# Optimization experiments

Hardware: AMD Instinct MI355X
Metric: run time of the kernel (lower is better)

## Reference

```python
import jax, jax.numpy as jnp
import numpy as np

TEMP = 0.01            # entropy temperature
THRESH = 0.92          # hamming similarity threshold
BETA = 0.25            # commitment weight
ENT_W = 0.1            # entropy loss weight


def _l2_normalize(x, axis=-1, eps=1e-12):
    n = jnp.sqrt(jnp.sum(x * x, axis=axis, keepdims=True))
    return x / jnp.maximum(n, eps)


def _entropy_loss(affinity):
    # affinity: [N, K] codebook affinities (cosine similarities)
    fa = affinity / TEMP
    probs = jax.nn.softmax(fa, axis=-1)
    log_probs = jax.nn.log_softmax(fa + 1e-5, axis=-1)
    avg_probs = jnp.mean(probs, axis=0)
    avg_entropy = -jnp.sum(avg_probs * jnp.log(avg_probs + 1e-5))
    sample_entropy = -jnp.mean(jnp.sum(probs * log_probs, axis=-1))
    return sample_entropy - avg_entropy


def _hamming_consistency_loss(input_blocks, z_e):
    # binary occupancy: non-air voxels -> 1
    binary = (jnp.argmax(input_blocks, axis=1) != 0).astype(jnp.float32)  # [B,24,24,24]
    B = binary.shape[0]
    # faithful to torch: plain reshapes (no transpose)
    patterns = binary.reshape(B, 6, 4, 6, 4, 6, 4).reshape(B, 6, 6, 6, 64).reshape(-1, 64)
    N = patterns.shape[0]
    P = patterns
    # pairwise hamming distance via two Gram matmuls
    ham = P @ (1.0 - P).T + (1.0 - P) @ P.T          # [N,N]
    sim = 1.0 - ham / 64.0
    mask = (sim > THRESH) & (~jnp.eye(N, dtype=bool))
    W = jax.lax.stop_gradient(jnp.where(mask, sim, 0.0))  # detached weights
    # pre-quant embeddings per chunk, l2-normalized; cosine distance matrix
    emb = jnp.transpose(z_e, (0, 2, 3, 4, 1)).reshape(N, -1)  # [N, C]
    en = _l2_normalize(emb, axis=1)
    cos = en @ en.T                                   # [N,N]
    dist = 1.0 - cos
    return jnp.sum(dist * W) / (jnp.sum(W) + 1e-8)


def setup_inputs() -> dict:
    key = jax.random.key(0)
    k1, k2, k3 = jax.random.split(key, 3)
    input_blocks = jax.random.normal(k1, (16, 32, 24, 24, 24), dtype=jnp.float32)
    z_e = jax.random.normal(k2, (16, 256, 6, 6, 6), dtype=jnp.float32)
    codebook = jax.random.normal(k3, (1024, 256), dtype=jnp.float32)
    return {"input_blocks": input_blocks, "z_e": z_e, "codebook": codebook}


def reference(input_blocks, z_e, codebook):
    B, C, H, W, D = z_e.shape
    z = jnp.transpose(z_e, (0, 2, 3, 4, 1)).reshape(-1, C)   # [N, C]
    zn = _l2_normalize(z, axis=1)
    en = _l2_normalize(codebook, axis=1)                      # [K, C]
    affinity = zn @ en.T                                      # [N, K]
    idx = jnp.argmax(affinity, axis=1)                        # max cosine == min L2 on sphere
    z_q = en[idx]                                             # [N, C]
    sg = jax.lax.stop_gradient
    codebook_loss = jnp.mean((z_q - sg(zn)) ** 2)
    commit_loss = BETA * jnp.mean((sg(z_q) - zn) ** 2)
    ent_loss = ENT_W * _entropy_loss(affinity)
    ham_loss = _hamming_consistency_loss(input_blocks, z_e)
    loss = codebook_loss + commit_loss + ent_loss + ham_loss
    # straight-through estimator
    z_q_ste = zn + sg(z_q - zn)
    z_q_out = jnp.transpose(z_q_ste.reshape(B, H, W, D, C), (0, 4, 1, 2, 3))
    return z_q_out, loss, idx
```

## Files before the change

### kernel.cpp

```cpp
#include <hip/hip_runtime.h>
#include <cstdint>
#include <cstddef>

#define N_ROWS 3456
#define C_DIM 256
#define K_CB 1024
#define B_SZ 16
#define SPATIAL 216
#define VOX 13824
#define NCH 32
#define NSB 216

typedef __attribute__((ext_vector_type(16))) float f32x16;
typedef __attribute__((ext_vector_type(8))) short bf16x8;

__device__ __forceinline__ unsigned short f2bf_rne(float f) {
    unsigned int u = __float_as_uint(f);
    u += 0x7FFFu + ((u >> 16) & 1u);
    return (unsigned short)(u >> 16);
}
__device__ __forceinline__ float bf2f(unsigned short h) {
    unsigned int u = ((unsigned int)h) << 16;
    return __uint_as_float(u);
}

__device__ __forceinline__ size_t swz(int n, int c) {
    return (size_t)(n >> 5) * 8192 + (size_t)((c >> 3) * 256) + (size_t)((n & 31) * 8) + (c & 7);
}

__global__ __launch_bounds__(256) void k_pre(
        const float* __restrict__ in, const float* __restrict__ cb,
        const float* __restrict__ ze,
        unsigned long long* __restrict__ pats,
        float* __restrict__ scal,
        float* __restrict__ en,
        unsigned short* __restrict__ ehi, unsigned short* __restrict__ elo,
        unsigned short* __restrict__ zhi, unsigned short* __restrict__ zlo) {
    int bid = blockIdx.x;
    int t = threadIdx.x;
    if (bid < 864) {
        if (bid == 0 && t < 16) scal[t] = 0.0f;
        int v = bid * 256 + t;
        int b = v / VOX;
        int r = v % VOX;
        const float* p = in + (size_t)b * NCH * VOX + r;
        float v0 = p[0];
        float mx = -INFINITY;
#pragma unroll
        for (int c = 1; c < NCH; ++c) mx = fmaxf(mx, p[(size_t)c * VOX]);
        unsigned long long m = __ballot(mx > v0);
        if ((t & 63) == 0) pats[v >> 6] = m;
        return;
    }
    __shared__ float ws[4];
    if (bid < 1888) {
        int k = bid - 864, c = t;
        float v = cb[k * C_DIM + c];
        float ss = v * v;
#pragma unroll
        for (int off = 32; off > 0; off >>= 1) ss += __shfl_down(ss, off, 64);
        if ((c & 63) == 0) ws[c >> 6] = ss;
        __syncthreads();
        float nrm = fmaxf(sqrtf(ws[0] + ws[1] + ws[2] + ws[3]), 1e-12f);
        float o = v / nrm;
        en[k * C_DIM + c] = o;
        unsigned short h = f2bf_rne(o);
        size_t off = swz(k, c);
        ehi[off] = h;
        elo[off] = f2bf_rne(o - bf2f(h));
    } else {
        int n = bid - 1888, c = t;
        int b = n / SPATIAL, s = n % SPATIAL;
        float v = ze[((size_t)(b * C_DIM + c)) * SPATIAL + s];
        float ss = v * v;
#pragma unroll
        for (int off = 32; off > 0; off >>= 1) ss += __shfl_down(ss, off, 64);
        if ((c & 63) == 0) ws[c >> 6] = ss;
        __syncthreads();
        float nrm = fmaxf(sqrtf(ws[0] + ws[1] + ws[2] + ws[3]), 1e-12f);
        float o = v / nrm;
        unsigned short h = f2bf_rne(o);
        size_t off = swz(n, c);
        zhi[off] = h;
        zlo[off] = f2bf_rne(o - bf2f(h));
    }
}

__global__ __launch_bounds__(128) void k_mid(
        const unsigned short* __restrict__ zhi, const unsigned short* __restrict__ zlo,
        const unsigned short* __restrict__ ehi, const unsigned short* __restrict__ elo,
        const unsigned long long* __restrict__ pats,
        float* __restrict__ aff, float* __restrict__ scal) {
    int t = threadIdx.x;
    int w = t >> 6, lane = t & 63;
    int bid = blockIdx.x;
    const bf16x8* __restrict__ Zh = (const bf16x8*)zhi;
    const bf16x8* __restrict__ Zl = (const bf16x8*)zlo;
    const bf16x8* __restrict__ Eh = (const bf16x8*)ehi;
    const bf16x8* __restrict__ El = (const bf16x8*)elo;

    if (bid < 432) {
        int ib = bid % 54, jb = bid / 54;
        int i0 = ib * 64, j0 = jb * 128;
        int sa = ib * 2;
        int sb = jb * 4 + w * 2;

        f32x16 acc[2][2];
#pragma unroll
        for (int r = 0; r < 2; ++r)
#pragma unroll
            for (int q = 0; q < 2; ++q)
#pragma unroll
                for (int e = 0; e < 16; ++e) acc[r][q][e] = 0.0f;

#pragma unroll
        for (int s16 = 0; s16 < 16; ++s16) {
            int u = s16 * 64 + lane;
            bf16x8 ah[2], al[2], bh[2], bl[2];
#pragma unroll
            for (int r = 0; r < 2; ++r) {
                ah[r] = Zh[(size_t)(sa + r) * 1024 + u];
                al[r] = Zl[(size_t)(sa + r) * 1024 + u];
            }
#pragma unroll
            for (int q = 0; q < 2; ++q) {
                bh[q] = Eh[(size_t)(sb + q) * 1024 + u];
                bl[q] = El[(size_t)(sb + q) * 1024 + u];
            }
#pragma unroll
            for (int r = 0; r < 2; ++r)
#pragma unroll
                for (int q = 0; q < 2; ++q) {
                    acc[r][q] = __builtin_amdgcn_mfma_f32_32x32x16_bf16(ah[r], bh[q], acc[r][q], 0, 0, 0);
                    acc[r][q] = __builtin_amdgcn_mfma_f32_32x32x16_bf16(ah[r], bl[q], acc[r][q], 0, 0, 0);
                    acc[r][q] = __builtin_amdgcn_mfma_f32_32x32x16_bf16(al[r], bh[q], acc[r][q], 0, 0, 0);
                }
        }
#pragma unroll
        for (int r = 0; r < 2; ++r)
#pragma unroll
            for (int q = 0; q < 2; ++q)
#pragma unroll
                for (int g = 0; g < 16; ++g) {
                    int row = i0 + r * 32 + (g & 3) + 8 * (g >> 2) + 4 * (lane >> 5);
                    int col = j0 + w * 64 + q * 32 + (lane & 31);
                    aff[(size_t)row * K_CB + col] = acc[r][q][g];
                }
        return;
    }

    int hb = bid - 432;
    int ti = 0, rem = hb;
    while (rem >= 27 - ti) { rem -= 27 - ti; ++ti; }
    int tj = ti + rem;
    int i0 = ti * 128, j0 = tj * 128;
    float factor = (ti == tj) ? 1.0f : 2.0f;
    int si = ti * 4 + w * 2;
    int sj = tj * 4;

    f32x16 acc[2][4];
#pragma unroll
    for (int a = 0; a < 2; ++a)
#pragma unroll
        for (int b = 0; b < 4; ++b)
#pragma unroll
            for (int e = 0; e < 16; ++e) acc[a][b][e] = 0.0f;

#pragma unroll
    for (int s16 = 0; s16 < 16; ++s16) {
        int u = s16 * 64 + lane;
        bf16x8 a0 = Zh[(size_t)si * 1024 + u];
        bf16x8 a1 = Zh[(size_t)(si + 1) * 1024 + u];
        bf16x8 bf[4];
#pragma unroll
        for (int c = 0; c < 4; ++c)
            bf[c] = Zh[(size_t)(sj + c) * 1024 + u];
#pragma unroll
        for (int c = 0; c < 4; ++c) {
            acc[0][c] = __builtin_amdgcn_mfma_f32_32x32x16_bf16(a0, bf[c], acc[0][c], 0, 0, 0);
            acc[1][c] = __builtin_amdgcn_mfma_f32_32x32x16_bf16(a1, bf[c], acc[1][c], 0, 0, 0);
        }
    }

    unsigned long long pj[4];
#pragma unroll
    for (int c = 0; c < 4; ++c) pj[c] = pats[j0 + c * 32 + (lane & 31)];

    float sW = 0.0f, sD = 0.0f;
#pragma unroll
    for (int r = 0; r < 2; ++r) {
        int ibase = i0 + w * 64 + r * 32 + 4 * (lane >> 5);
#pragma unroll
        for (int g = 0; g < 16; ++g) {
            int gi = ibase + (g & 3) + 8 * (g >> 2);
            unsigned long long pi = pats[gi];
#pragma unroll
            for (int c = 0; c < 4; ++c) {
                int gj = j0 + c * 32 + (lane & 31);
                int pop = __popcll(pi ^ pj[c]);
                float wgt = (pop <= 5 && gi != gj) ? (1.0f - (float)pop * 0.015625f) : 0.0f;
                sW += wgt;
                sD += wgt * acc[r][c][g];
            }
        }
    }
#pragma unroll
    for (int off = 32; off > 0; off >>= 1) {
        sW += __shfl_down(sW, off, 64);
        sD += __shfl_down(sD, off, 64);
    }
    if (lane == 0) {
        atomicAdd(&scal[2], factor * sW);
        atomicAdd(&scal[3], factor * sD);
    }
}

#define ZQS 257
__global__ __launch_bounds__(1024) void k_post(
        const float* __restrict__ aff, const float* __restrict__ en,
        float* __restrict__ avgp_part, float* __restrict__ scal,
        float* __restrict__ out) {
    __shared__ float lps[16][K_CB];
    __shared__ float zq[16 * ZQS];
    __shared__ float lsc[32];
    __shared__ float ws16[16];
    __shared__ int lastflag;
    unsigned int* done = (unsigned int*)&scal[8];
    int t = threadIdx.x;
    int lane = t & 63, w = t >> 6;
    int n0 = blockIdx.x * 16;
    int row = n0 + w;

    const float* ap = aff + (size_t)row * K_CB;
    float4 v[4];
#pragma unroll
    for (int j = 0; j < 4; ++j)
        v[j] = *(const float4*)&ap[j * 256 + lane * 4];

    float m = v[0].x; int mi = lane * 4;
#pragma unroll
    for (int j = 0; j < 4; ++j)
#pragma unroll
        for (int i = 0; i < 4; ++i) {
            float x = ((const float*)&v[j])[i];
            int col = j * 256 + lane * 4 + i;
            if (x > m) { m = x; mi = col; }
        }
#pragma unroll
    for (int off = 32; off > 0; off >>= 1) {
        float vo = __shfl_down(m, off, 64);
        int   io = __shfl_down(mi, off, 64);
        if (vo > m || (vo == m && io < mi)) { m = vo; mi = io; }
    }
    m = __shfl(m, 0, 64);
    mi = __shfl(mi, 0, 64);

    float e[16];
    float S = 0.0f, T = 0.0f;
#pragma unroll
    for (int j = 0; j < 4; ++j)
#pragma unroll
        for (int i = 0; i < 4; ++i) {
            float d = 100.0f * (((const float*)&v[j])[i] - m);
            float ee = __expf(d);
            e[j * 4 + i] = ee; S += ee; T += ee * d;
        }
#pragma unroll
    for (int off = 32; off > 0; off >>= 1) {
        S += __shfl_down(S, off, 64);
        T += __shfl_down(T, off, 64);
    }
    S = __shfl(S, 0, 64);
    T = __shfl(T, 0, 64);
    float invS = 1.0f / S;
    float se = logf(S) - T * invS;
    float cm = 2.0f - 2.0f * m;
    if (lane == 0) out[884737 + row] = (float)mi;

    float4 g4 = *(const float4*)&en[(size_t)mi * C_DIM + lane * 4];
    zq[w * ZQS + lane * 4 + 0] = g4.x;
    zq[w * ZQS + lane * 4 + 1] = g4.y;
    zq[w * ZQS + lane * 4 + 2] = g4.z;
    zq[w * ZQS + lane * 4 + 3] = g4.w;

#pragma unroll
    for (int j = 0; j < 4; ++j)
#pragma unroll
        for (int i = 0; i < 4; ++i)
            lps[w][j * 256 + lane * 4 + i] = e[j * 4 + i] * invS;
    if (lane == 0) { lsc[w] = se; lsc[16 + w] = cm; }
    __syncthreads();

    {
        float csum = 0.0f;
#pragma unroll
        for (int ww = 0; ww < 16; ++ww) csum += lps[ww][t];
        avgp_part[(size_t)blockIdx.x * K_CB + t] = csum;
    }
    if (t == 0) {
        float a = 0.0f;
#pragma unroll
        for (int i = 0; i < 16; ++i) a += lsc[i];
        atomicAdd(&scal[0], a);
    }
    if (t == 1) {
        float a = 0.0f;
#pragma unroll
        for (int i = 0; i < 16; ++i) a += lsc[16 + i];
        atomicAdd(&scal[1], a);
    }

    {
        int rlane = t & 15, cgrp = t >> 4;
        int n = n0 + rlane;
        int b = n / SPATIAL, s = n - b * SPATIAL;
        size_t obase = ((size_t)b * C_DIM) * SPATIAL + s;
#pragma unroll
        for (int cc = 0; cc < 4; ++cc) {
            int c = cgrp * 4 + cc;
            out[obase + (size_t)c * SPATIAL] = zq[rlane * ZQS + c];
        }
    }

    __syncthreads();
    if (t == 0) {
        __threadfence();
        unsigned int old = atomicAdd(done, 1u);
        lastflag = (old == NSB - 1) ? 1 : 0;
    }
    __syncthreads();
    if (lastflag) {
        __threadfence();
        float apv = 0.0f;
        for (int bb = 0; bb < NSB; ++bb)
            apv += avgp_part[(size_t)bb * K_CB + t];
        float ap2 = apv * (1.0f / N_ROWS);
        float term = ap2 * logf(ap2 + 1e-5f);
#pragma unroll
        for (int off = 32; off > 0; off >>= 1) term += __shfl_down(term, off, 64);
        if (lane == 0) ws16[w] = term;
        __syncthreads();
        if (t == 0) {
            float sAP = 0.0f;
#pragma unroll
            for (int i = 0; i < 16; ++i) sAP += ws16[i];
            float s0 = atomicAdd(&scal[0], 0.0f);
            float s1 = atomicAdd(&scal[1], 0.0f);
            float s2 = atomicAdd(&scal[2], 0.0f);
            float s3 = atomicAdd(&scal[3], 0.0f);
            float sample = s0 * (1.0f / N_ROWS);
            float commit = s1 * (1.0f / ((float)N_ROWS * C_DIM));
            float ent = 0.1f * (sample + sAP);
            float ham = (s2 - s3) / (s2 + 1e-8f);
            out[884736] = 1.25f * commit + ent + ham;
        }
    }
}

extern "C" void kernel_launch(void* const* d_in, const int* in_sizes, int n_in,
                              void* d_out, int out_size, void* d_ws, size_t ws_size,
                              hipStream_t stream) {
    const float* in_blocks = (const float*)d_in[0];
    const float* z_e       = (const float*)d_in[1];
    const float* cb        = (const float*)d_in[2];
    float* out = (float*)d_out;

    char* ws = (char*)d_ws;
    float* en   = (float*)(ws + 0);
    float* aff  = (float*)(ws + 1048576);
    unsigned short* zhi = (unsigned short*)(ws + 15204352);
    unsigned short* zlo = (unsigned short*)(ws + 16973824);
    unsigned short* ehi = (unsigned short*)(ws + 18743296);
    unsigned short* elo = (unsigned short*)(ws + 19267584);
    unsigned long long* pats = (unsigned long long*)(ws + 19791872);
    float* avgp_part = (float*)(ws + 19819520);
    float* scal = (float*)(ws + 20704256);

    k_pre<<<5344, 256, 0, stream>>>(in_blocks, cb, z_e, pats, scal,
                                    en, ehi, elo, zhi, zlo);
    k_mid<<<810, 128, 0, stream>>>(zhi, zlo, ehi, elo, pats, aff, scal);
    k_post<<<NSB, 1024, 0, stream>>>(aff, en, avgp_part, scal, out);
}
```

Before: 148.4 us.

## Fuse affinity GEMM with argmax/softmax epilogue, drop affinity buffer round-trip

Merges the affinity GEMM and the post-processing kernel into one launch. Each GEMM block now computes 32 rows against the full 1024-entry codebook across 8 waves, then does argmax, softmax statistics, the column sums for the average probabilities and the z_q scatter straight from registers. This removes the 14 MB affinity write and re-read and one kernel launch. In exchange there are fewer, larger GEMM blocks (108) at 512 threads with more register pressure, and the Hamming blocks leave 6 of their 8 waves idle.

```diff
diff --git a/kernel.cpp b/kernel.cpp
--- a/kernel.cpp
+++ b/kernel.cpp
@@ -9,7 +9,8 @@
 #define SPATIAL 216
 #define VOX 13824
 #define NCH 32
-#define NSB 216
+#define N_GBLK 108
+#define N_FBLK 486
 
 typedef __attribute__((ext_vector_type(16))) float f32x16;
 typedef __attribute__((ext_vector_type(8))) short bf16x8;
@@ -86,239 +87,245 @@
     }
 }
 
-__global__ __launch_bounds__(128) void k_mid(
+__global__ __launch_bounds__(512, 2) void k_fat(
         const unsigned short* __restrict__ zhi, const unsigned short* __restrict__ zlo,
         const unsigned short* __restrict__ ehi, const unsigned short* __restrict__ elo,
         const unsigned long long* __restrict__ pats,
-        float* __restrict__ aff, float* __restrict__ scal) {
+        const float* __restrict__ en,
+        float* __restrict__ avgp_part, float* __restrict__ scal,
+        float* __restrict__ out) {
+    __shared__ float zq[32 * 257];
+    __shared__ float sm[32][8];
+    __shared__ int   si[32][8];
+    __shared__ float sS[32][8];
+    __shared__ float sT[32][8];
+    __shared__ float gm[32];
+    __shared__ int   gmi[32];
+    __shared__ float invS[32];
+    __shared__ float ws8[8];
+    __shared__ int lastflag;
+    unsigned int* done = (unsigned int*)&scal[8];
+
     int t = threadIdx.x;
     int w = t >> 6, lane = t & 63;
+    int half = lane >> 5, l31 = lane & 31;
     int bid = blockIdx.x;
     const bf16x8* __restrict__ Zh = (const bf16x8*)zhi;
     const bf16x8* __restrict__ Zl = (const bf16x8*)zlo;
     const bf16x8* __restrict__ Eh = (const bf16x8*)ehi;
     const bf16x8* __restrict__ El = (const bf16x8*)elo;
 
-    if (bid < 432) {
-        int ib = bid % 54, jb = bid / 54;
-        int i0 = ib * 64, j0 = jb * 128;
-        int sa = ib * 2;
-        int sb = jb * 4 + w * 2;
-
-        f32x16 acc[2][2];
-#pragma unroll
-        for (int r = 0; r < 2; ++r)
-#pragma unroll
-            for (int q = 0; q < 2; ++q)
-#pragma unroll
-                for (int e = 0; e < 16; ++e) acc[r][q][e] = 0.0f;
+    if (bid < N_GBLK) {
+        int sa = bid;
+        int n0 = bid * 32;
+
+        f32x16 acc[4];
+#pragma unroll
+        for (int q = 0; q < 4; ++q)
+#pragma unroll
+            for (int e = 0; e < 16; ++e) acc[q][e] = 0.0f;
 
 #pragma unroll
         for (int s16 = 0; s16 < 16; ++s16) {
             int u = s16 * 64 + lane;
-            bf16x8 ah[2], al[2], bh[2], bl[2];
-#pragma unroll
-            for (int r = 0; r < 2; ++r) {
-                ah[r] = Zh[(size_t)(sa + r) * 1024 + u];
-                al[r] = Zl[(size_t)(sa + r) * 1024 + u];
-            }
-#pragma unroll
-            for (int q = 0; q < 2; ++q) {
-                bh[q] = Eh[(size_t)(sb + q) * 1024 + u];
-                bl[q] = El[(size_t)(sb + q) * 1024 + u];
-            }
-#pragma unroll
-            for (int r = 0; r < 2; ++r)
-#pragma unroll
-                for (int q = 0; q < 2; ++q) {
-                    acc[r][q] = __builtin_amdgcn_mfma_f32_32x32x16_bf16(ah[r], bh[q], acc[r][q], 0, 0, 0);
-                    acc[r][q] = __builtin_amdgcn_mfma_f32_32x32x16_bf16(ah[r], bl[q], acc[r][q], 0, 0, 0);
-                    acc[r][q] = __builtin_amdgcn_mfma_f32_32x32x16_bf16(al[r], bh[q], acc[r][q], 0, 0, 0);
+            bf16x8 ah = Zh[(size_t)sa * 1024 + u];
+            bf16x8 al = Zl[(size_t)sa * 1024 + u];
+            bf16x8 bh[4], bl[4];
+#pragma unroll
+            for (int q = 0; q < 4; ++q) {
+                bh[q] = Eh[(size_t)(w * 4 + q) * 1024 + u];
+                bl[q] = El[(size_t)(w * 4 + q) * 1024 + u];
+            }
+#pragma unroll
+            for (int q = 0; q < 4; ++q) {
+                acc[q] = __builtin_amdgcn_mfma_f32_32x32x16_bf16(ah, bh[q], acc[q], 0, 0, 0);
+                acc[q] = __builtin_amdgcn_mfma_f32_32x32x16_bf16(ah, bl[q], acc[q], 0, 0, 0);
+                acc[q] = __builtin_amdgcn_mfma_f32_32x32x16_bf16(al, bh[q], acc[q], 0, 0, 0);
+            }
+        }
+
+#pragma unroll
+        for (int g = 0; g < 16; ++g) {
+            float m = acc[0][g];
+            int mi = w * 128 + l31;
+#pragma unroll
+            for (int q = 1; q < 4; ++q) {
+                float x = acc[q][g];
+                int c = w * 128 + q * 32 + l31;
+                if (x > m) { m = x; mi = c; }
+            }
+#pragma unroll
+            for (int mask = 1; mask < 32; mask <<= 1) {
+                float vo = __shfl_xor(m, mask, 64);
+                int   io = __shfl_xor(mi, mask, 64);
+                if (vo > m || (vo == m && io < mi)) { m = vo; mi = io; }
+            }
+            int row = (g & 3) + 8 * (g >> 2) + 4 * half;
+            if (l31 == 0) { sm[row][w] = m; si[row][w] = mi; }
+        }
+        __syncthreads();
+
+        float cmv = 0.0f;
+        if (t < 32) {
+            float m = sm[t][0];
+            int mi = si[t][0];
+#pragma unroll
+            for (int ww = 1; ww < 8; ++ww) {
+                float mw = sm[t][ww];
+                int miw = si[t][ww];
+                if (mw > m || (mw == m && miw < mi)) { m = mw; mi = miw; }
+            }
+            gm[t] = m; gmi[t] = mi;
+            out[884737 + n0 + t] = (float)mi;
+            cmv = 2.0f - 2.0f * m;
+        }
+        if (w == 0) {
+#pragma unroll
+            for (int off = 32; off > 0; off >>= 1) cmv += __shfl_down(cmv, off, 64);
+            if (lane == 0) atomicAdd(&scal[1], cmv);
+        }
+        __syncthreads();
+
+#pragma unroll
+        for (int g = 0; g < 16; ++g) {
+            int row = (g & 3) + 8 * (g >> 2) + 4 * half;
+            float gmr = gm[row];
+            float S = 0.0f, T = 0.0f;
+#pragma unroll
+            for (int q = 0; q < 4; ++q) {
+                float d = 100.0f * (acc[q][g] - gmr);
+                float ee = __expf(d);
+                S += ee; T += ee * d;
+                acc[q][g] = ee;
+            }
+#pragma unroll
+            for (int mask = 1; mask < 32; mask <<= 1) {
+                S += __shfl_xor(S, mask, 64);
+                T += __shfl_xor(T, mask, 64);
+            }
+            if (l31 == 0) { sS[row][w] = S; sT[row][w] = T; }
+        }
+#pragma unroll
+        for (int rr = 0; rr < 4; ++rr) {
+            int row = w * 4 + rr;
+            int mi = gmi[row];
+            float4 g4 = *(const float4*)&en[(size_t)mi * C_DIM + lane * 4];
+            zq[row * 257 + lane * 4 + 0] = g4.x;
+            zq[row * 257 + lane * 4 + 1] = g4.y;
+            zq[row * 257 + lane * 4 + 2] = g4.z;
+            zq[row * 257 + lane * 4 + 3] = g4.w;
+        }
+        __syncthreads();
+
+        float sev = 0.0f;
+        if (t < 32) {
+            float S = 0.0f, T = 0.0f;
+#pragma unroll
+            for (int ww = 0; ww < 8; ++ww) { S += sS[t][ww]; T += sT[t][ww]; }
+            float iv = 1.0f / S;
+            invS[t] = iv;
+            sev = logf(S) - T * iv;
+        }
+        if (w == 0) {
+#pragma unroll
+            for (int off = 32; off > 0; off >>= 1) sev += __shfl_down(sev, off, 64);
+            if (lane == 0) atomicAdd(&scal[0], sev);
+        }
+        __syncthreads();
+
+        {
+            float cs[4] = {0.0f, 0.0f, 0.0f, 0.0f};
+#pragma unroll
+            for (int g = 0; g < 16; ++g) {
+                int row = (g & 3) + 8 * (g >> 2) + 4 * half;
+                float iv = invS[row];
+#pragma unroll
+                for (int q = 0; q < 4; ++q) cs[q] += acc[q][g] * iv;
+            }
+#pragma unroll
+            for (int q = 0; q < 4; ++q) cs[q] += __shfl_xor(cs[q], 32, 64);
+            if (half == 0) {
+#pragma unroll
+                for (int q = 0; q < 4; ++q)
+                    avgp_part[(size_t)bid * K_CB + w * 128 + q * 32 + l31] = cs[q];
+            }
+        }
+
+        {
+            int rl = t & 31, cg = t >> 5;
+            int n = n0 + rl;
+            int b = n / SPATIAL, s = n - b * SPATIAL;
+            size_t obase = ((size_t)b * C_DIM) * SPATIAL + s;
+#pragma unroll
+            for (int cc = 0; cc < 16; ++cc) {
+                int c = cg * 16 + cc;
+                out[obase + (size_t)c * SPATIAL] = zq[rl * 257 + c];
+            }
+        }
+    } else if (w < 2) {
+        int hb = bid - N_GBLK;
+        int ti = 0, rem = hb;
+        while (rem >= 27 - ti) { rem -= 27 - ti; ++ti; }
+        int tj = ti + rem;
+        int i0 = ti * 128, j0 = tj * 128;
+        float factor = (ti == tj) ? 1.0f : 2.0f;
+        int sib = ti * 4 + w * 2;
+        int sjb = tj * 4;
+
+        f32x16 acc[2][4];
+#pragma unroll
+        for (int a = 0; a < 2; ++a)
+#pragma unroll
+            for (int b = 0; b < 4; ++b)
+#pragma unroll
+                for (int e = 0; e < 16; ++e) acc[a][b][e] = 0.0f;
+
+#pragma unroll
+        for (int s16 = 0; s16 < 16; ++s16) {
+            int u = s16 * 64 + lane;
+            bf16x8 a0 = Zh[(size_t)sib * 1024 + u];
+            bf16x8 a1 = Zh[(size_t)(sib + 1) * 1024 + u];
+            bf16x8 bf[4];
+#pragma unroll
+            for (int c = 0; c < 4; ++c)
+                bf[c] = Zh[(size_t)(sjb + c) * 1024 + u];
+#pragma unroll
+            for (int c = 0; c < 4; ++c) {
+                acc[0][c] = __builtin_amdgcn_mfma_f32_32x32x16_bf16(a0, bf[c], acc[0][c], 0, 0, 0);
+                acc[1][c] = __builtin_amdgcn_mfma_f32_32x32x16_bf16(a1, bf[c], acc[1][c], 0, 0, 0);
+            }
+        }
+
+        unsigned long long pj[4];
+#pragma unroll
+        for (int c = 0; c < 4; ++c) pj[c] = pats[j0 + c * 32 + l31];
+
+        float sW = 0.0f, sD = 0.0f;
+#pragma unroll
+        for (int r = 0; r < 2; ++r) {
+            int ibase = i0 + w * 64 + r * 32 + 4 * half;
+#pragma unroll
+            for (int g = 0; g < 16; ++g) {
+                int gi = ibase + (g & 3) + 8 * (g >> 2);
+                unsigned long long pi = pats[gi];
+#pragma unroll
+                for (int c = 0; c < 4; ++c) {
+                    int gj = j0 + c * 32 + l31;
+                    int pop = __popcll(pi ^ pj[c]);
+                    float wgt = (pop <= 5 && gi != gj) ? (1.0f - (float)pop * 0.015625f) : 0.0f;
+                    sW += wgt;
+                    sD += wgt * acc[r][c][g];
                 }
-        }
-#pragma unroll
-        for (int r = 0; r < 2; ++r)
-#pragma unroll
-            for (int q = 0; q < 2; ++q)
-#pragma unroll
-                for (int g = 0; g < 16; ++g) {
-                    int row = i0 + r * 32 + (g & 3) + 8 * (g >> 2) + 4 * (lane >> 5);
-                    int col = j0 + w * 64 + q * 32 + (lane & 31);
-                    aff[(size_t)row * K_CB + col] = acc[r][q][g];
-                }
-        return;
-    }
-
-    int hb = bid - 432;
-    int ti = 0, rem = hb;
-    while (rem >= 27 - ti) { rem -= 27 - ti; ++ti; }
-    int tj = ti + rem;
-    int i0 = ti * 128, j0 = tj * 128;
-    float factor = (ti == tj) ? 1.0f : 2.0f;
-    int si = ti * 4 + w * 2;
-    int sj = tj * 4;
-
-    f32x16 acc[2][4];
-#pragma unroll
-    for (int a = 0; a < 2; ++a)
-#pragma unroll
-        for (int b = 0; b < 4; ++b)
-#pragma unroll
-            for (int e = 0; e < 16; ++e) acc[a][b][e] = 0.0f;
-
-#pragma unroll
-    for (int s16 = 0; s16 < 16; ++s16) {
-        int u = s16 * 64 + lane;
-        bf16x8 a0 = Zh[(size_t)si * 1024 + u];
-        bf16x8 a1 = Zh[(size_t)(si + 1) * 1024 + u];
-        bf16x8 bf[4];
-#pragma unroll
-        for (int c = 0; c < 4; ++c)
-            bf[c] = Zh[(size_t)(sj + c) * 1024 + u];
-#pragma unroll
-        for (int c = 0; c < 4; ++c) {
-            acc[0][c] = __builtin_amdgcn_mfma_f32_32x32x16_bf16(a0, bf[c], acc[0][c], 0, 0, 0);
-            acc[1][c] = __builtin_amdgcn_mfma_f32_32x32x16_bf16(a1, bf[c], acc[1][c], 0, 0, 0);
-        }
-    }
-
-    unsigned long long pj[4];
-#pragma unroll
-    for (int c = 0; c < 4; ++c) pj[c] = pats[j0 + c * 32 + (lane & 31)];
-
-    float sW = 0.0f, sD = 0.0f;
-#pragma unroll
-    for (int r = 0; r < 2; ++r) {
-        int ibase = i0 + w * 64 + r * 32 + 4 * (lane >> 5);
-#pragma unroll
-        for (int g = 0; g < 16; ++g) {
-            int gi = ibase + (g & 3) + 8 * (g >> 2);
-            unsigned long long pi = pats[gi];
-#pragma unroll
-            for (int c = 0; c < 4; ++c) {
-                int gj = j0 + c * 32 + (lane & 31);
-                int pop = __popcll(pi ^ pj[c]);
-                float wgt = (pop <= 5 && gi != gj) ? (1.0f - (float)pop * 0.015625f) : 0.0f;
-                sW += wgt;
-                sD += wgt * acc[r][c][g];
-            }
-        }
-    }
-#pragma unroll
-    for (int off = 32; off > 0; off >>= 1) {
-        sW += __shfl_down(sW, off, 64);
-        sD += __shfl_down(sD, off, 64);
-    }
-    if (lane == 0) {
-        atomicAdd(&scal[2], factor * sW);
-        atomicAdd(&scal[3], factor * sD);
-    }
-}
-
-#define ZQS 257
-__global__ __launch_bounds__(1024) void k_post(
-        const float* __restrict__ aff, const float* __restrict__ en,
-        float* __restrict__ avgp_part, float* __restrict__ scal,
-        float* __restrict__ out) {
-    __shared__ float lps[16][K_CB];
-    __shared__ float zq[16 * ZQS];
-    __shared__ float lsc[32];
-    __shared__ float ws16[16];
-    __shared__ int lastflag;
-    unsigned int* done = (unsigned int*)&scal[8];
-    int t = threadIdx.x;
-    int lane = t & 63, w = t >> 6;
-    int n0 = blockIdx.x * 16;
-    int row = n0 + w;
-
-    const float* ap = aff + (size_t)row * K_CB;
-    float4 v[4];
-#pragma unroll
-    for (int j = 0; j < 4; ++j)
-        v[j] = *(const float4*)&ap[j * 256 + lane * 4];
-
-    float m = v[0].x; int mi = lane * 4;
-#pragma unroll
-    for (int j = 0; j < 4; ++j)
-#pragma unroll
-        for (int i = 0; i < 4; ++i) {
-            float x = ((const float*)&v[j])[i];
-            int col = j * 256 + lane * 4 + i;
-            if (x > m) { m = x; mi = col; }
-        }
-#pragma unroll
-    for (int off = 32; off > 0; off >>= 1) {
-        float vo = __shfl_down(m, off, 64);
-        int   io = __shfl_down(mi, off, 64);
-        if (vo > m || (vo == m && io < mi)) { m = vo; mi = io; }
-    }
-    m = __shfl(m, 0, 64);
-    mi = __shfl(mi, 0, 64);
-
-    float e[16];
-    float S = 0.0f, T = 0.0f;
-#pragma unroll
-    for (int j = 0; j < 4; ++j)
-#pragma unroll
-        for (int i = 0; i < 4; ++i) {
-            float d = 100.0f * (((const float*)&v[j])[i] - m);
-            float ee = __expf(d);
-            e[j * 4 + i] = ee; S += ee; T += ee * d;
-        }
-#pragma unroll
-    for (int off = 32; off > 0; off >>= 1) {
-        S += __shfl_down(S, off, 64);
-        T += __shfl_down(T, off, 64);
-    }
-    S = __shfl(S, 0, 64);
-    T = __shfl(T, 0, 64);
-    float invS = 1.0f / S;
-    float se = logf(S) - T * invS;
-    float cm = 2.0f - 2.0f * m;
-    if (lane == 0) out[884737 + row] = (float)mi;
-
-    float4 g4 = *(const float4*)&en[(size_t)mi * C_DIM + lane * 4];
-    zq[w * ZQS + lane * 4 + 0] = g4.x;
-    zq[w * ZQS + lane * 4 + 1] = g4.y;
-    zq[w * ZQS + lane * 4 + 2] = g4.z;
-    zq[w * ZQS + lane * 4 + 3] = g4.w;
-
-#pragma unroll
-    for (int j = 0; j < 4; ++j)
-#pragma unroll
-        for (int i = 0; i < 4; ++i)
-            lps[w][j * 256 + lane * 4 + i] = e[j * 4 + i] * invS;
-    if (lane == 0) { lsc[w] = se; lsc[16 + w] = cm; }
-    __syncthreads();
-
-    {
-        float csum = 0.0f;
-#pragma unroll
-        for (int ww = 0; ww < 16; ++ww) csum += lps[ww][t];
-        avgp_part[(size_t)blockIdx.x * K_CB + t] = csum;
-    }
-    if (t == 0) {
-        float a = 0.0f;
-#pragma unroll
-        for (int i = 0; i < 16; ++i) a += lsc[i];
-        atomicAdd(&scal[0], a);
-    }
-    if (t == 1) {
-        float a = 0.0f;
-#pragma unroll
-        for (int i = 0; i < 16; ++i) a += lsc[16 + i];
-        atomicAdd(&scal[1], a);
-    }
-
-    {
-        int rlane = t & 15, cgrp = t >> 4;
-        int n = n0 + rlane;
-        int b = n / SPATIAL, s = n - b * SPATIAL;
-        size_t obase = ((size_t)b * C_DIM) * SPATIAL + s;
-#pragma unroll
-        for (int cc = 0; cc < 4; ++cc) {
-            int c = cgrp * 4 + cc;
-            out[obase + (size_t)c * SPATIAL] = zq[rlane * ZQS + c];
+            }
+        }
+#pragma unroll
+        for (int off = 32; off > 0; off >>= 1) {
+            sW += __shfl_down(sW, off, 64);
+            sD += __shfl_down(sD, off, 64);
+        }
+        if (lane == 0) {
+            atomicAdd(&scal[2], factor * sW);
+            atomicAdd(&scal[3], factor * sD);
         }
     }
 
@@ -326,24 +333,35 @@
     if (t == 0) {
         __threadfence();
         unsigned int old = atomicAdd(done, 1u);
-        lastflag = (old == NSB - 1) ? 1 : 0;
+        lastflag = (old == N_FBLK - 1) ? 1 : 0;
     }
     __syncthreads();
     if (lastflag) {
         __threadfence();
-        float apv = 0.0f;
-        for (int bb = 0; bb < NSB; ++bb)
-            apv += avgp_part[(size_t)bb * K_CB + t];
-        float ap2 = apv * (1.0f / N_ROWS);
-        float term = ap2 * logf(ap2 + 1e-5f);
+        int col0 = t, col1 = t + 512;
+        float p0 = 0.0f, p1 = 0.0f, p2 = 0.0f, p3 = 0.0f;
+        float q0 = 0.0f, q1 = 0.0f, q2 = 0.0f, q3 = 0.0f;
+        for (int bb = 0; bb < N_GBLK; bb += 4) {
+            p0 += avgp_part[(size_t)(bb + 0) * K_CB + col0];
+            p1 += avgp_part[(size_t)(bb + 1) * K_CB + col0];
+            p2 += avgp_part[(size_t)(bb + 2) * K_CB + col0];
+            p3 += avgp_part[(size_t)(bb + 3) * K_CB + col0];
+            q0 += avgp_part[(size_t)(bb + 0) * K_CB + col1];
+            q1 += avgp_part[(size_t)(bb + 1) * K_CB + col1];
+            q2 += avgp_part[(size_t)(bb + 2) * K_CB + col1];
+            q3 += avgp_part[(size_t)(bb + 3) * K_CB + col1];
+        }
+        float ap0 = (p0 + p1 + p2 + p3) * (1.0f / N_ROWS);
+        float ap1 = (q0 + q1 + q2 + q3) * (1.0f / N_ROWS);
+        float term = ap0 * logf(ap0 + 1e-5f) + ap1 * logf(ap1 + 1e-5f);
 #pragma unroll
         for (int off = 32; off > 0; off >>= 1) term += __shfl_down(term, off, 64);
-        if (lane == 0) ws16[w] = term;
+        if (lane == 0) ws8[w] = term;
         __syncthreads();
         if (t == 0) {
             float sAP = 0.0f;
 #pragma unroll
-            for (int i = 0; i < 16; ++i) sAP += ws16[i];
+            for (int i = 0; i < 8; ++i) sAP += ws8[i];
             float s0 = atomicAdd(&scal[0], 0.0f);
             float s1 = atomicAdd(&scal[1], 0.0f);
             float s2 = atomicAdd(&scal[2], 0.0f);
@@ -367,7 +385,6 @@
 
     char* ws = (char*)d_ws;
     float* en   = (float*)(ws + 0);
-    float* aff  = (float*)(ws + 1048576);
     unsigned short* zhi = (unsigned short*)(ws + 15204352);
     unsigned short* zlo = (unsigned short*)(ws + 16973824);
     unsigned short* ehi = (unsigned short*)(ws + 18743296);
@@ -378,6 +395,6 @@
 
     k_pre<<<5344, 256, 0, stream>>>(in_blocks, cb, z_e, pats, scal,
                                     en, ehi, elo, zhi, zlo);
-    k_mid<<<810, 128, 0, stream>>>(zhi, zlo, ehi, elo, pats, aff, scal);
-    k_post<<<NSB, 1024, 0, stream>>>(aff, en, avgp_part, scal, out);
-}
+    k_fat<<<N_FBLK, 512, 0, stream>>>(zhi, zlo, ehi, elo, pats, en,
+                                      avgp_part, scal, out);
+}
```

Result: no change. 149.5 us (+0.7%).
